# Kernel optimization log

Hardware: AMD Instinct MI355X
Metric: run time of the kernel (lower is better)

The kernel has to match this reference:

```python
import jax, jax.numpy as jnp
import numpy as np

DIM = 128
NUM_HEADS = 8
HEAD_DIM = DIM // NUM_HEADS
SCALE = HEAD_DIM ** -0.5


def _attn_branch(xs, Wq, bq, Wp, bp):
    # xs: (N, L, C) batch of sequences; Q=K=V=q (per the module)
    N, L, C = xs.shape
    q = xs @ Wq + bq                                   # (N, L, C)
    q = q.reshape(N, L, NUM_HEADS, HEAD_DIM).transpose(0, 2, 1, 3)  # (N, h, L, d)
    qs = q * SCALE
    attn = jax.nn.softmax(jnp.einsum('nhld,nhmd->nhlm', qs, qs), axis=-1)
    out = jnp.einsum('nhlm,nhmd->nhld', attn, q)       # (N, h, L, d)
    out = out.transpose(0, 2, 1, 3).reshape(N, L, C)
    return out @ Wp + bp


def setup_inputs() -> dict:
    key = jax.random.key(0)
    ks = jax.random.split(key, 12)
    B, C, D, H, W = 1, DIM, 31, 32, 32
    s = 0.02
    return {
        'x': jax.random.normal(ks[0], (B, C, D, H, W), jnp.float32),
        'Wq_spec': jax.random.normal(ks[1], (C, C), jnp.float32) * s,
        'bq_spec': jnp.zeros((C,), jnp.float32),
        'Wp_spec': jax.random.normal(ks[2], (C, C), jnp.float32) * s,
        'bp_spec': jnp.zeros((C,), jnp.float32),
        'Wq_spat': jax.random.normal(ks[3], (C, C), jnp.float32) * s,
        'bq_spat': jnp.zeros((C,), jnp.float32),
        'Wp_spat': jax.random.normal(ks[4], (C, C), jnp.float32) * s,
        'bp_spat': jnp.zeros((C,), jnp.float32),
        'Wg': jax.random.normal(ks[5], (2 * C, C), jnp.float32) * s,
        'bg': jnp.zeros((C,), jnp.float32),
    }


def reference(x, Wq_spec, bq_spec, Wp_spec, bp_spec,
              Wq_spat, bq_spat, Wp_spat, bp_spat, Wg, bg):
    B, C, D, H, W = x.shape
    # ---- spectral branch: sequences of length D per spatial position ----
    x_spec = x.transpose(0, 3, 4, 2, 1).reshape(B * H * W, D, C)
    out_spec = _attn_branch(x_spec, Wq_spec, bq_spec, Wp_spec, bp_spec)
    out_spectral = out_spec.reshape(B, H, W, D, C).transpose(0, 4, 3, 1, 2)  # (B,C,D,H,W)
    # ---- spatial branch: sequences of length H*W per band ----
    x_spat = x.transpose(0, 2, 3, 4, 1).reshape(B * D, H * W, C)
    out_spat = _attn_branch(x_spat, Wq_spat, bq_spat, Wp_spat, bp_spat)
    out_spatial = out_spat.reshape(B, D, H, W, C).transpose(0, 4, 1, 2, 3)   # (B,C,D,H,W)
    # ---- sigmoid-gated fusion (global average pooled gate) ----
    gi = jnp.concatenate([
        out_spectral.mean(axis=(2, 3, 4)),
        out_spatial.mean(axis=(2, 3, 4)),
    ], axis=-1)                                          # (B, 2C)
    gate = jax.nn.sigmoid(gi @ Wg + bg)[:, :, None, None, None]  # (B,C,1,1,1)
    return gate * out_spectral + (1.0 - gate) * out_spatial
```

## Files before the change

### kernel.cpp

```cpp
#include <hip/hip_runtime.h>
#include <cstddef>

#define CC 128
#define NH 8
#define HD 16
#define DDIM 31
#define HWW 1024
#define TOK 31744
#define SCALE2 0.0625f
#define QTOK 64

typedef __attribute__((ext_vector_type(4))) short  short4v;
typedef __attribute__((ext_vector_type(8))) short  short8v;
typedef __attribute__((ext_vector_type(4))) float  float4v;
typedef __attribute__((ext_vector_type(2))) unsigned uint2v;
typedef __attribute__((ext_vector_type(8))) __bf16 bf16x8;

__device__ inline unsigned bf16rne(float f) {
    unsigned u = __float_as_uint(f);
    return (u + 0x7fffu + ((u >> 16) & 1u)) >> 16;
}
__device__ inline float bf2f(unsigned h) { return __uint_as_float(h << 16); }

__device__ inline unsigned packsplit(float v) {
    unsigned h = bf16rne(v);
    unsigned l = bf16rne(v - bf2f(h));
    return h | (l << 16);
}
__device__ inline uint2 pack_hi4(uint4 p) {
    return make_uint2((p.x & 0xffffu) | (p.y << 16),
                      (p.z & 0xffffu) | (p.w << 16));
}
__device__ inline uint2 pack_lo4(uint4 p) {
    return make_uint2((p.x >> 16) | (p.y & 0xffff0000u),
                      (p.z >> 16) | (p.w & 0xffff0000u));
}

__device__ inline short4v pack_pf(unsigned u0, unsigned u1,
                                  unsigned u2, unsigned u3) {
    uint2v pd;
    pd[0] = __builtin_amdgcn_perm(u1, u0, 0x07060302u);
    pd[1] = __builtin_amdgcn_perm(u3, u2, 0x07060302u);
    return __builtin_bit_cast(short4v, pd);
}

__device__ inline float4v mfma32(short8v a, short8v b, float4v c) {
    return __builtin_amdgcn_mfma_f32_16x16x32_bf16(
        __builtin_bit_cast(bf16x8, a), __builtin_bit_cast(bf16x8, b), c, 0, 0, 0);
}

__device__ inline void load_wfrags32(const float* __restrict__ W, int co0, int l,
                                     int quad, short8v* ah, short8v* al)
{
#pragma unroll
    for (int k4 = 0; k4 < 4; ++k4) {
#pragma unroll
        for (int j = 0; j < 8; ++j) {
            float w = W[(size_t)(k4 * 32 + quad * 8 + j) * CC + co0 + l];
            unsigned h = bf16rne(w);
            ah[k4][j] = (short)h;
            al[k4][j] = (short)bf16rne(w - bf2f(h));
        }
    }
}

#define AST 136

__global__ __launch_bounds__(512, 4) void qproj_kernel(
    const float* __restrict__ x,
    const float* __restrict__ Wq1, const float* __restrict__ Wq2,
    const float* __restrict__ bq1, const float* __restrict__ bq2,
    unsigned* __restrict__ q1p, unsigned* __restrict__ q2p,
    float* __restrict__ sums)
{
    __shared__ ushort sbuf[2 * QTOK * AST];
    ushort* Ahi = sbuf;
    ushort* Alo = sbuf + QTOK * AST;
    unsigned* S = (unsigned*)sbuf;
    const int tid = threadIdx.x;
    const int t0  = blockIdx.x * QTOK;
    if (blockIdx.x == 0 && tid < 2 * CC) sums[tid] = 0.f;

    for (int i = tid; i < QTOK * 32; i += 512) {
        int t = i & 63, c4 = i >> 6;
        unsigned hw[2], lw[2];
#pragma unroll
        for (int p = 0; p < 2; ++p) {
            unsigned h0, l0, h1, l1;
            {
                float v = x[(size_t)(c4 * 4 + p * 2 + 0) * TOK + t0 + t];
                h0 = bf16rne(v); l0 = bf16rne(v - bf2f(h0));
            }
            {
                float v = x[(size_t)(c4 * 4 + p * 2 + 1) * TOK + t0 + t];
                h1 = bf16rne(v); l1 = bf16rne(v - bf2f(h1));
            }
            hw[p] = h0 | (h1 << 16);
            lw[p] = l0 | (l1 << 16);
        }
        *(uint2*)&Ahi[t * AST + c4 * 4] = make_uint2(hw[0], hw[1]);
        *(uint2*)&Alo[t * AST + c4 * 4] = make_uint2(lw[0], lw[1]);
    }
    __syncthreads();

    const int lane = tid & 63;
    const int l    = lane & 15;
    const int quad = lane >> 4;
    const int co0  = (tid >> 6) * 16;

    short8v ah[2][4], al[2][4];
    load_wfrags32(Wq1, co0, l, quad, ah[0], al[0]);
    load_wfrags32(Wq2, co0, l, quad, ah[1], al[1]);
    float4v acc[2][4];
#pragma unroll
    for (int br = 0; br < 2; ++br)
#pragma unroll
        for (int nt = 0; nt < 4; ++nt) acc[br][nt] = (float4v){0.f, 0.f, 0.f, 0.f};
#pragma unroll
    for (int k4 = 0; k4 < 4; ++k4) {
#pragma unroll
        for (int nt = 0; nt < 4; ++nt) {
            short8v bh = *(const short8v*)&Ahi[(nt * 16 + l) * AST + k4 * 32 + quad * 8];
            short8v bl = *(const short8v*)&Alo[(nt * 16 + l) * AST + k4 * 32 + quad * 8];
            acc[0][nt] = mfma32(ah[0][k4], bh, acc[0][nt]);
            acc[0][nt] = mfma32(ah[0][k4], bl, acc[0][nt]);
            acc[0][nt] = mfma32(al[0][k4], bh, acc[0][nt]);
            acc[1][nt] = mfma32(ah[1][k4], bh, acc[1][nt]);
            acc[1][nt] = mfma32(ah[1][k4], bl, acc[1][nt]);
            acc[1][nt] = mfma32(al[1][k4], bh, acc[1][nt]);
        }
    }

    for (int branch = 0; branch < 2; ++branch) {
        const float* bq = branch ? bq2 : bq1;
        unsigned* op    = branch ? q2p : q1p;
        float4 bv = *(const float4*)&bq[co0 + quad * 4];
        float bb[4] = {bv.x, bv.y, bv.z, bv.w};
        __syncthreads();
#pragma unroll
        for (int nt = 0; nt < 4; ++nt) {
#pragma unroll
            for (int reg = 0; reg < 4; ++reg)
                S[(nt * 16 + l) * AST + co0 + quad * 4 + reg] =
                    packsplit(acc[branch][nt][reg] + bb[reg]);
        }
        __syncthreads();
        for (int i = tid; i < QTOK * 32; i += 512) {
            int t = i >> 5, c4 = i & 31;
            uint4 pv = *(const uint4*)&S[t * AST + c4 * 4];
            *(uint4*)&op[(size_t)(t0 + t) * CC + c4 * 4] = pv;
        }
    }
}

#define QS2 132
#define QSS 20
#define QTP 1044
__global__ __launch_bounds__(1024, 4) void attn_kernel(
    unsigned* __restrict__ q1p, unsigned* __restrict__ q2p,
    float* __restrict__ sums)
{
    __shared__ __align__(16) ushort smem[HWW * QSS + HD * QTP];
    __shared__ float fsum[CC];
    const int tid  = threadIdx.x;
    const int lane = tid & 63;
    const int l    = lane & 15;
    const int quad = lane >> 4;
    const float k2 = SCALE2 * 1.44269504f;
    const short4v onesb = {(short)0x3F80, (short)0x3F80, (short)0x3F80, (short)0x3F80};
    if (tid < CC) fsum[tid] = 0.f;

    {
        const int d = blockIdx.x >> 3, h = blockIdx.x & 7;
        ushort* Qs  = smem;
        ushort* QTs = smem + HWW * QSS;
        const size_t base = (size_t)d * HWW * CC + h * HD;

        for (int i = tid; i < HWW * 4; i += 1024) {
            int row = i >> 2, q4 = i & 3;
            uint4 p = *(const uint4*)&q2p[base + (size_t)row * CC + q4 * 4];
            *(uint2*)&Qs[row * QSS + q4 * 4] = pack_hi4(p);
            QTs[(q4 * 4 + 0) * QTP + row] = (ushort)p.x;
            QTs[(q4 * 4 + 1) * QTP + row] = (ushort)p.y;
            QTs[(q4 * 4 + 2) * QTP + row] = (ushort)p.z;
            QTs[(q4 * 4 + 3) * QTP + row] = (ushort)p.w;
        }
        __syncthreads();

        const int Rw = (tid >> 6) * 64;
        short4v qf[4];
#pragma unroll
        for (int lt = 0; lt < 4; ++lt) {
            short4v raw = *(short4v*)&Qs[(Rw + lt * 16 + l) * QSS + quad * 4];
            short4v sc;
#pragma unroll
            for (int e = 0; e < 4; ++e) {
                float f = bf2f((unsigned)(ushort)raw[e]) * k2;
                sc[e] = (short)bf16rne(f);
            }
            qf[lt] = sc;
        }

        float4v acc[4], accs[4];
#pragma unroll
        for (int lt = 0; lt < 4; ++lt) {
            acc[lt]  = (float4v){0.f, 0.f, 0.f, 0.f};
            accs[lt] = (float4v){0.f, 0.f, 0.f, 0.f};
        }

#pragma unroll 2
        for (int mt = 0; mt < 64; ++mt) {
            const int m0 = mt * 16;
            short4v ka = *(short4v*)&Qs[(m0 + l) * QSS + quad * 4];
            short4v vb = *(short4v*)&QTs[l * QTP + m0 + quad * 4];
#pragma unroll
            for (int lt = 0; lt < 4; ++lt) {
                float4v s = __builtin_amdgcn_mfma_f32_16x16x16bf16_1k(
                    ka, qf[lt], (float4v){0.f, 0.f, 0.f, 0.f}, 0, 0, 0);
                unsigned u0 = __float_as_uint(__builtin_amdgcn_exp2f(s[0]));
                unsigned u1 = __float_as_uint(__builtin_amdgcn_exp2f(s[1]));
                unsigned u2 = __float_as_uint(__builtin_amdgcn_exp2f(s[2]));
                unsigned u3 = __float_as_uint(__builtin_amdgcn_exp2f(s[3]));
                short4v pf = pack_pf(u0, u1, u2, u3);
                acc[lt]  = __builtin_amdgcn_mfma_f32_16x16x16bf16_1k(vb, pf, acc[lt], 0, 0, 0);
                accs[lt] = __builtin_amdgcn_mfma_f32_16x16x16bf16_1k(onesb, pf, accs[lt], 0, 0, 0);
            }
        }

        float vsum[4] = {0.f, 0.f, 0.f, 0.f};
#pragma unroll
        for (int lt = 0; lt < 4; ++lt) {
            float inv = 1.f / accs[lt][0];
            int token = Rw + lt * 16 + l;
            float v0 = acc[lt][0] * inv, v1 = acc[lt][1] * inv;
            float v2 = acc[lt][2] * inv, v3 = acc[lt][3] * inv;
            uint4 pv;
            pv.x = packsplit(v0); pv.y = packsplit(v1);
            pv.z = packsplit(v2); pv.w = packsplit(v3);
            *(uint4*)&q2p[base + (size_t)token * CC + quad * 4] = pv;
            vsum[0] += v0; vsum[1] += v1; vsum[2] += v2; vsum[3] += v3;
        }
#pragma unroll
        for (int reg = 0; reg < 4; ++reg) {
            float v = vsum[reg];
            v += __shfl_xor(v, 1); v += __shfl_xor(v, 2);
            v += __shfl_xor(v, 4); v += __shfl_xor(v, 8);
            if (l == 0) atomicAdd(&fsum[quad * 4 + reg], v);
        }
        __syncthreads();
        if (tid < HD) atomicAdd(&sums[CC + h * HD + tid], fsum[tid]);
    }

    const int half_id = blockIdx.x >> 1;
    const bool has_job = (blockIdx.x & 1) ? (half_id < 4) : (half_id < 124);
    if (!has_job) return;
    const int job = (blockIdx.x & 1) ? (124 + half_id) : half_id;
    const int hw0 = job * 8;

    __syncthreads();
    if (tid < CC) fsum[tid] = 0.f;

    const int wave = tid >> 6;
    const int hwl  = wave >> 1;
    const int half = wave & 1;
    const int hw   = hw0 + hwl;
    ushort* Q = smem + hwl * (32 * QS2);
    for (int it = 0; it < 8; ++it) {
        int idx = it * 64 + lane;
        int dd = half * 16 + (idx >> 5), c4 = idx & 31;
        if (dd < 31) {
            uint4 p = *(const uint4*)&q1p[((size_t)dd * HWW + hw) * CC + c4 * 4];
            *(uint2*)&Q[dd * QS2 + c4 * 4] = pack_hi4(p);
        }
    }
    if (half) for (int i = lane; i < 128; i += 64) Q[31 * QS2 + i] = 0;
    __syncthreads();

    const int hh = half * 4;
#pragma unroll
    for (int hl = 0; hl < 4; ++hl) {
        const int hc = (hh + hl) * HD;
        short4v qf[2];
        qf[0] = *(const short4v*)&Q[l * QS2 + hc + quad * 4];
        qf[1] = *(const short4v*)&Q[(16 + l) * QS2 + hc + quad * 4];
        short4v va[2];
#pragma unroll
        for (int j = 0; j < 2; ++j)
#pragma unroll
            for (int jj = 0; jj < 4; ++jj)
                va[j][jj] = (short)Q[(j * 16 + quad * 4 + jj) * QS2 + hc + l];

        float4v o[2]   = {(float4v){0.f,0.f,0.f,0.f}, (float4v){0.f,0.f,0.f,0.f}};
        float4v osr[2] = {(float4v){0.f,0.f,0.f,0.f}, (float4v){0.f,0.f,0.f,0.f}};
#pragma unroll
        for (int j = 0; j < 2; ++j) {
#pragma unroll
            for (int i2 = 0; i2 < 2; ++i2) {
                float4v s = __builtin_amdgcn_mfma_f32_16x16x16bf16_1k(
                    qf[j], qf[i2], (float4v){0.f,0.f,0.f,0.f}, 0, 0, 0);
                unsigned u0 = __float_as_uint(__builtin_amdgcn_exp2f(s[0] * k2));
                unsigned u1 = __float_as_uint(__builtin_amdgcn_exp2f(s[1] * k2));
                unsigned u2 = __float_as_uint(__builtin_amdgcn_exp2f(s[2] * k2));
                unsigned u3 = __float_as_uint(__builtin_amdgcn_exp2f(s[3] * k2));
                if (j == 1 && quad == 3) u3 = 0;
                short4v pf = pack_pf(u0, u1, u2, u3);
                o[i2]   = __builtin_amdgcn_mfma_f32_16x16x16bf16_1k(va[j], pf, o[i2], 0, 0, 0);
                osr[i2] = __builtin_amdgcn_mfma_f32_16x16x16bf16_1k(onesb, pf, osr[i2], 0, 0, 0);
            }
        }
        float vsum[4] = {0.f, 0.f, 0.f, 0.f};
#pragma unroll
        for (int i2 = 0; i2 < 2; ++i2) {
            float inv = 1.f / osr[i2][0];
            int dq = i2 * 16 + l;
            if (dq < 31) {
                uint4 pv;
                float v0 = o[i2][0] * inv, v1 = o[i2][1] * inv;
                float v2 = o[i2][2] * inv, v3 = o[i2][3] * inv;
                pv.x = packsplit(v0); pv.y = packsplit(v1);
                pv.z = packsplit(v2); pv.w = packsplit(v3);
                *(uint4*)&q1p[((size_t)dq * HWW + hw) * CC + hc + quad * 4] = pv;
                vsum[0] += v0; vsum[1] += v1; vsum[2] += v2; vsum[3] += v3;
            }
        }
#pragma unroll
        for (int r = 0; r < 4; ++r) {
            float v = vsum[r];
            v += __shfl_xor(v, 1); v += __shfl_xor(v, 2);
            v += __shfl_xor(v, 4); v += __shfl_xor(v, 8);
            if (l == 0) atomicAdd(&fsum[hc + quad * 4 + r], v);
        }
    }
    __syncthreads();
    if (tid < CC) atomicAdd(&sums[tid], fsum[tid]);
}

__global__ __launch_bounds__(512, 4) void oproj_kernel(
    const unsigned* __restrict__ q1p, const unsigned* __restrict__ q2p,
    const float* __restrict__ Wp1, const float* __restrict__ Wp2,
    const float* __restrict__ bp1, const float* __restrict__ bp2,
    const float* __restrict__ Wg,  const float* __restrict__ bg,
    const float* __restrict__ sums, float* __restrict__ out)
{
    __shared__ ushort sbuf[2 * 64 * AST];
    ushort* Ahi = sbuf;
    ushort* Alo = sbuf + 64 * AST;
    unsigned* S = (unsigned*)sbuf;
    __shared__ float pa[4][CC];
    __shared__ float giv[2 * CC];
    __shared__ float gf[CC];
    const int tid = threadIdx.x;
    const int t0  = blockIdx.x * 64;
    const int lane = tid & 63;
    const int l    = lane & 15;
    const int quad = lane >> 4;
    const int co0  = (tid >> 6) * 16;

    {
        const int part = tid >> 7, c = tid & 127;
        const float* Wp = (part < 2) ? Wp1 : Wp2;
        const float* sp = (part < 2) ? sums : sums + CC;
        const int k0 = (part & 1) * 64;
        float a = 0.f;
        for (int kk = 0; kk < 64; ++kk) {
            int k = k0 + kk;
            a += sp[k] * Wp[(size_t)k * CC + c];
        }
        pa[part][c] = a;
        __syncthreads();
        if (tid < 2 * CC) {
            float m = (tid < CC) ? (pa[0][tid] + pa[1][tid])
                                 : (pa[2][tid - CC] + pa[3][tid - CC]);
            float bb = (tid < CC) ? bp1[tid] : bp2[tid - CC];
            giv[tid] = m * (1.f / (float)TOK) + bb;
        }
        __syncthreads();
        float b = 0.f;
        for (int kk = 0; kk < 64; ++kk) {
            int j = part * 64 + kk;
            b += giv[j] * Wg[(size_t)j * CC + c];
        }
        pa[part][c] = b;
        __syncthreads();
        if (tid < CC)
            gf[tid] = 1.f / (1.f + __expf(-(bg[tid] + pa[0][tid] + pa[1][tid] +
                                           pa[2][tid] + pa[3][tid])));
    }

    float4v acc[2][4];
#pragma unroll
    for (int br = 0; br < 2; ++br)
#pragma unroll
        for (int nt = 0; nt < 4; ++nt) acc[br][nt] = (float4v){0.f, 0.f, 0.f, 0.f};

    for (int br = 0; br < 2; ++br) {
        const unsigned* Ap = br ? q2p : q1p;
        const float*    W  = br ? Wp2 : Wp1;
        short8v ah[4], al[4];
        load_wfrags32(W, co0, l, quad, ah, al);
        __syncthreads();
        for (int i = tid; i < 64 * 32; i += 512) {
            int t = i >> 5, c4 = i & 31;
            uint4 p = *(const uint4*)&Ap[(size_t)(t0 + t) * CC + c4 * 4];
            *(uint2*)&Ahi[t * AST + c4 * 4] = pack_hi4(p);
            *(uint2*)&Alo[t * AST + c4 * 4] = pack_lo4(p);
        }
        __syncthreads();
#pragma unroll
        for (int k4 = 0; k4 < 4; ++k4) {
#pragma unroll
            for (int nt = 0; nt < 4; ++nt) {
                short8v bh = *(const short8v*)&Ahi[(nt * 16 + l) * AST + k4 * 32 + quad * 8];
                short8v bl = *(const short8v*)&Alo[(nt * 16 + l) * AST + k4 * 32 + quad * 8];
                acc[br][nt] = mfma32(ah[k4], bh, acc[br][nt]);
                acc[br][nt] = mfma32(ah[k4], bl, acc[br][nt]);
                acc[br][nt] = mfma32(al[k4], bh, acc[br][nt]);
            }
        }
    }

    float4 b1 = *(const float4*)&bp1[co0 + quad * 4];
    float4 b2 = *(const float4*)&bp2[co0 + quad * 4];
    float bb1[4] = {b1.x, b1.y, b1.z, b1.w};
    float bb2[4] = {b2.x, b2.y, b2.z, b2.w};
    float gg[4];
#pragma unroll
    for (int e = 0; e < 4; ++e) gg[e] = gf[co0 + quad * 4 + e];

    __syncthreads();
#pragma unroll
    for (int nt = 0; nt < 4; ++nt) {
        int tl = nt * 16 + l;
#pragma unroll
        for (int reg = 0; reg < 4; ++reg) {
            float v = gg[reg] * (acc[0][nt][reg] + bb1[reg]) +
                      (1.f - gg[reg]) * (acc[1][nt][reg] + bb2[reg]);
            S[(co0 + quad * 4 + reg) * 66 + tl] = __float_as_uint(v);
        }
    }
    __syncthreads();
    for (int i = tid; i < 128 * 32; i += 512) {
        int co = i >> 5, t2 = i & 31;
        uint2 v = *(const uint2*)&S[co * 66 + t2 * 2];
        *(uint2*)&out[(size_t)co * TOK + t0 + t2 * 2] = v;
    }
}

extern "C" void kernel_launch(void* const* d_in, const int* in_sizes, int n_in,
                              void* d_out, int out_size, void* d_ws, size_t ws_size,
                              hipStream_t stream)
{
    const float* x   = (const float*)d_in[0];
    const float* Wq1 = (const float*)d_in[1];
    const float* bq1 = (const float*)d_in[2];
    const float* Wp1 = (const float*)d_in[3];
    const float* bp1 = (const float*)d_in[4];
    const float* Wq2 = (const float*)d_in[5];
    const float* bq2 = (const float*)d_in[6];
    const float* Wp2 = (const float*)d_in[7];
    const float* bp2 = (const float*)d_in[8];
    const float* Wg  = (const float*)d_in[9];
    const float* bg  = (const float*)d_in[10];
    float* out = (float*)d_out;

    const size_t plane = (size_t)TOK * CC;
    unsigned* q1p = (unsigned*)d_ws;
    unsigned* q2p = q1p + plane;
    float*   sums = (float*)(q2p + plane);

    const size_t need = 2 * plane * sizeof(unsigned) + 2 * CC * sizeof(float);
    if (ws_size < need) return;

    qproj_kernel<<<dim3(TOK / QTOK), 512, 0, stream>>>(x, Wq1, Wq2, bq1, bq2,
                                                       q1p, q2p, sums);
    attn_kernel<<<dim3(248), 1024, 0, stream>>>(q1p, q2p, sums);
    oproj_kernel<<<dim3(496), 512, 0, stream>>>(q1p, q2p,
                                                Wp1, Wp2, bp1, bp2, Wg, bg,
                                                sums, out);
}
```

Before: 172.0 us.

## Store Q projections as bf16-only buffers and split attention blocks by branch

The Q projection now writes only the high bf16 half into separate 16-bit workspace buffers, where it used to write packed hi/lo pairs. This halves the bytes qproj stores and attn reads, since attention only ever used the high part. The attention kernel no longer runs both branches in every block. It launches 376 blocks: the first 128 handle spectral sequences and the rest handle spatial ones, which removes the uneven tail job assignment. The cost is extra workspace for the two new buffers, and each block now does a single, shorter task.

New measurement: 159.9 us. 7.1% less time.

```diff
diff --git a/kernel.cpp b/kernel.cpp
--- a/kernel.cpp
+++ b/kernel.cpp
@@ -70,13 +70,12 @@
     const float* __restrict__ x,
     const float* __restrict__ Wq1, const float* __restrict__ Wq2,
     const float* __restrict__ bq1, const float* __restrict__ bq2,
-    unsigned* __restrict__ q1p, unsigned* __restrict__ q2p,
+    ushort* __restrict__ qh1, ushort* __restrict__ qh2,
     float* __restrict__ sums)
 {
     __shared__ ushort sbuf[2 * QTOK * AST];
     ushort* Ahi = sbuf;
     ushort* Alo = sbuf + QTOK * AST;
-    unsigned* S = (unsigned*)sbuf;
     const int tid = threadIdx.x;
     const int t0  = blockIdx.x * QTOK;
     if (blockIdx.x == 0 && tid < 2 * CC) sums[tid] = 0.f;
@@ -131,25 +130,26 @@
         }
     }
 
-    for (int branch = 0; branch < 2; ++branch) {
-        const float* bq = branch ? bq2 : bq1;
-        unsigned* op    = branch ? q2p : q1p;
-        float4 bv = *(const float4*)&bq[co0 + quad * 4];
-        float bb[4] = {bv.x, bv.y, bv.z, bv.w};
-        __syncthreads();
-#pragma unroll
-        for (int nt = 0; nt < 4; ++nt) {
+    float4 bv1 = *(const float4*)&bq1[co0 + quad * 4];
+    float4 bv2 = *(const float4*)&bq2[co0 + quad * 4];
+    float bb[2][4] = {{bv1.x, bv1.y, bv1.z, bv1.w},
+                      {bv2.x, bv2.y, bv2.z, bv2.w}};
+    __syncthreads();
+#pragma unroll
+    for (int br = 0; br < 2; ++br)
+#pragma unroll
+        for (int nt = 0; nt < 4; ++nt)
 #pragma unroll
             for (int reg = 0; reg < 4; ++reg)
-                S[(nt * 16 + l) * AST + co0 + quad * 4 + reg] =
-                    packsplit(acc[branch][nt][reg] + bb[reg]);
-        }
-        __syncthreads();
-        for (int i = tid; i < QTOK * 32; i += 512) {
-            int t = i >> 5, c4 = i & 31;
-            uint4 pv = *(const uint4*)&S[t * AST + c4 * 4];
-            *(uint4*)&op[(size_t)(t0 + t) * CC + c4 * 4] = pv;
-        }
+                sbuf[br * (QTOK * AST) + (nt * 16 + l) * AST + co0 + quad * 4 + reg] =
+                    (ushort)bf16rne(acc[br][nt][reg] + bb[br][reg]);
+    __syncthreads();
+    for (int i = tid; i < 2 * QTOK * 16; i += 512) {
+        int br = i >> 10, j = i & 1023;
+        int t = j >> 4, c8 = j & 15;
+        ushort* op = br ? qh2 : qh1;
+        uint4 pv = *(const uint4*)&sbuf[br * (QTOK * AST) + t * AST + c8 * 8];
+        *(uint4*)&op[(size_t)(t0 + t) * CC + c8 * 8] = pv;
     }
 }
 
@@ -157,6 +157,7 @@
 #define QSS 20
 #define QTP 1044
 __global__ __launch_bounds__(1024, 4) void attn_kernel(
+    const ushort* __restrict__ qh1, const ushort* __restrict__ qh2,
     unsigned* __restrict__ q1p, unsigned* __restrict__ q2p,
     float* __restrict__ sums)
 {
@@ -170,20 +171,23 @@
     const short4v onesb = {(short)0x3F80, (short)0x3F80, (short)0x3F80, (short)0x3F80};
     if (tid < CC) fsum[tid] = 0.f;
 
-    {
-        const int d = blockIdx.x >> 3, h = blockIdx.x & 7;
+    if (blockIdx.x >= 128) {
+        const int sp = blockIdx.x - 128;
+        const int d = sp >> 3, h = sp & 7;
         ushort* Qs  = smem;
         ushort* QTs = smem + HWW * QSS;
-        const size_t base = (size_t)d * HWW * CC + h * HD;
+        const size_t baseh = (size_t)d * HWW * CC + h * HD;
+        const size_t base  = baseh;
 
         for (int i = tid; i < HWW * 4; i += 1024) {
             int row = i >> 2, q4 = i & 3;
-            uint4 p = *(const uint4*)&q2p[base + (size_t)row * CC + q4 * 4];
-            *(uint2*)&Qs[row * QSS + q4 * 4] = pack_hi4(p);
-            QTs[(q4 * 4 + 0) * QTP + row] = (ushort)p.x;
-            QTs[(q4 * 4 + 1) * QTP + row] = (ushort)p.y;
-            QTs[(q4 * 4 + 2) * QTP + row] = (ushort)p.z;
-            QTs[(q4 * 4 + 3) * QTP + row] = (ushort)p.w;
+            uint2 p = *(const uint2*)&qh2[baseh + (size_t)row * CC + q4 * 4];
+            *(uint2*)&Qs[row * QSS + q4 * 4] = p;
+            const ushort* ps = (const ushort*)&p;
+            QTs[(q4 * 4 + 0) * QTP + row] = ps[0];
+            QTs[(q4 * 4 + 1) * QTP + row] = ps[1];
+            QTs[(q4 * 4 + 2) * QTP + row] = ps[2];
+            QTs[(q4 * 4 + 3) * QTP + row] = ps[3];
         }
         __syncthreads();
 
@@ -249,90 +253,82 @@
         }
         __syncthreads();
         if (tid < HD) atomicAdd(&sums[CC + h * HD + tid], fsum[tid]);
-    }
-
-    const int half_id = blockIdx.x >> 1;
-    const bool has_job = (blockIdx.x & 1) ? (half_id < 4) : (half_id < 124);
-    if (!has_job) return;
-    const int job = (blockIdx.x & 1) ? (124 + half_id) : half_id;
-    const int hw0 = job * 8;
-
-    __syncthreads();
-    if (tid < CC) fsum[tid] = 0.f;
-
-    const int wave = tid >> 6;
-    const int hwl  = wave >> 1;
-    const int half = wave & 1;
-    const int hw   = hw0 + hwl;
-    ushort* Q = smem + hwl * (32 * QS2);
-    for (int it = 0; it < 8; ++it) {
-        int idx = it * 64 + lane;
-        int dd = half * 16 + (idx >> 5), c4 = idx & 31;
-        if (dd < 31) {
-            uint4 p = *(const uint4*)&q1p[((size_t)dd * HWW + hw) * CC + c4 * 4];
-            *(uint2*)&Q[dd * QS2 + c4 * 4] = pack_hi4(p);
-        }
-    }
-    if (half) for (int i = lane; i < 128; i += 64) Q[31 * QS2 + i] = 0;
-    __syncthreads();
-
-    const int hh = half * 4;
-#pragma unroll
-    for (int hl = 0; hl < 4; ++hl) {
-        const int hc = (hh + hl) * HD;
-        short4v qf[2];
-        qf[0] = *(const short4v*)&Q[l * QS2 + hc + quad * 4];
-        qf[1] = *(const short4v*)&Q[(16 + l) * QS2 + hc + quad * 4];
-        short4v va[2];
-#pragma unroll
-        for (int j = 0; j < 2; ++j)
-#pragma unroll
-            for (int jj = 0; jj < 4; ++jj)
-                va[j][jj] = (short)Q[(j * 16 + quad * 4 + jj) * QS2 + hc + l];
-
-        float4v o[2]   = {(float4v){0.f,0.f,0.f,0.f}, (float4v){0.f,0.f,0.f,0.f}};
-        float4v osr[2] = {(float4v){0.f,0.f,0.f,0.f}, (float4v){0.f,0.f,0.f,0.f}};
-#pragma unroll
-        for (int j = 0; j < 2; ++j) {
+    } else {
+        const int hw0 = blockIdx.x * 8;
+        const int wave = tid >> 6;
+        const int hwl  = wave >> 1;
+        const int half = wave & 1;
+        const int hw   = hw0 + hwl;
+        ushort* Q = smem + hwl * (32 * QS2);
+        for (int it = 0; it < 8; ++it) {
+            int idx = it * 64 + lane;
+            int dd = half * 16 + (idx >> 5), c4 = idx & 31;
+            if (dd < 31) {
+                uint2 p = *(const uint2*)&qh1[((size_t)dd * HWW + hw) * CC + c4 * 4];
+                *(uint2*)&Q[dd * QS2 + c4 * 4] = p;
+            }
+        }
+        if (half) for (int i = lane; i < 128; i += 64) Q[31 * QS2 + i] = 0;
+        __syncthreads();
+
+        const int hh = half * 4;
+#pragma unroll
+        for (int hl = 0; hl < 4; ++hl) {
+            const int hc = (hh + hl) * HD;
+            short4v qf[2];
+            qf[0] = *(const short4v*)&Q[l * QS2 + hc + quad * 4];
+            qf[1] = *(const short4v*)&Q[(16 + l) * QS2 + hc + quad * 4];
+            short4v va[2];
+#pragma unroll
+            for (int j = 0; j < 2; ++j)
+#pragma unroll
+                for (int jj = 0; jj < 4; ++jj)
+                    va[j][jj] = (short)Q[(j * 16 + quad * 4 + jj) * QS2 + hc + l];
+
+            float4v o[2]   = {(float4v){0.f,0.f,0.f,0.f}, (float4v){0.f,0.f,0.f,0.f}};
+            float4v osr[2] = {(float4v){0.f,0.f,0.f,0.f}, (float4v){0.f,0.f,0.f,0.f}};
+#pragma unroll
+            for (int j = 0; j < 2; ++j) {
+#pragma unroll
+                for (int i2 = 0; i2 < 2; ++i2) {
+                    float4v s = __builtin_amdgcn_mfma_f32_16x16x16bf16_1k(
+                        qf[j], qf[i2], (float4v){0.f,0.f,0.f,0.f}, 0, 0, 0);
+                    unsigned u0 = __float_as_uint(__builtin_amdgcn_exp2f(s[0] * k2));
+                    unsigned u1 = __float_as_uint(__builtin_amdgcn_exp2f(s[1] * k2));
+                    unsigned u2 = __float_as_uint(__builtin_amdgcn_exp2f(s[2] * k2));
+                    unsigned u3 = __float_as_uint(__builtin_amdgcn_exp2f(s[3] * k2));
+                    if (j == 1 && quad == 3) u3 = 0;
+                    short4v pf = pack_pf(u0, u1, u2, u3);
+                    o[i2]   = __builtin_amdgcn_mfma_f32_16x16x16bf16_1k(va[j], pf, o[i2], 0, 0, 0);
+                    osr[i2] = __builtin_amdgcn_mfma_f32_16x16x16bf16_1k(onesb, pf, osr[i2], 0, 0, 0);
+                }
+            }
+            float vsum[4] = {0.f, 0.f, 0.f, 0.f};
 #pragma unroll
             for (int i2 = 0; i2 < 2; ++i2) {
-                float4v s = __builtin_amdgcn_mfma_f32_16x16x16bf16_1k(
-                    qf[j], qf[i2], (float4v){0.f,0.f,0.f,0.f}, 0, 0, 0);
-                unsigned u0 = __float_as_uint(__builtin_amdgcn_exp2f(s[0] * k2));
-                unsigned u1 = __float_as_uint(__builtin_amdgcn_exp2f(s[1] * k2));
-                unsigned u2 = __float_as_uint(__builtin_amdgcn_exp2f(s[2] * k2));
-                unsigned u3 = __float_as_uint(__builtin_amdgcn_exp2f(s[3] * k2));
-                if (j == 1 && quad == 3) u3 = 0;
-                short4v pf = pack_pf(u0, u1, u2, u3);
-                o[i2]   = __builtin_amdgcn_mfma_f32_16x16x16bf16_1k(va[j], pf, o[i2], 0, 0, 0);
-                osr[i2] = __builtin_amdgcn_mfma_f32_16x16x16bf16_1k(onesb, pf, osr[i2], 0, 0, 0);
-            }
-        }
-        float vsum[4] = {0.f, 0.f, 0.f, 0.f};
-#pragma unroll
-        for (int i2 = 0; i2 < 2; ++i2) {
-            float inv = 1.f / osr[i2][0];
-            int dq = i2 * 16 + l;
-            if (dq < 31) {
-                uint4 pv;
-                float v0 = o[i2][0] * inv, v1 = o[i2][1] * inv;
-                float v2 = o[i2][2] * inv, v3 = o[i2][3] * inv;
-                pv.x = packsplit(v0); pv.y = packsplit(v1);
-                pv.z = packsplit(v2); pv.w = packsplit(v3);
-                *(uint4*)&q1p[((size_t)dq * HWW + hw) * CC + hc + quad * 4] = pv;
-                vsum[0] += v0; vsum[1] += v1; vsum[2] += v2; vsum[3] += v3;
-            }
-        }
-#pragma unroll
-        for (int r = 0; r < 4; ++r) {
-            float v = vsum[r];
-            v += __shfl_xor(v, 1); v += __shfl_xor(v, 2);
-            v += __shfl_xor(v, 4); v += __shfl_xor(v, 8);
-            if (l == 0) atomicAdd(&fsum[hc + quad * 4 + r], v);
-        }
-    }
-    __syncthreads();
-    if (tid < CC) atomicAdd(&sums[tid], fsum[tid]);
+                float inv = 1.f / osr[i2][0];
+                int dq = i2 * 16 + l;
+                if (dq < 31) {
+                    uint4 pv;
+                    float v0 = o[i2][0] * inv, v1 = o[i2][1] * inv;
+                    float v2 = o[i2][2] * inv, v3 = o[i2][3] * inv;
+                    pv.x = packsplit(v0); pv.y = packsplit(v1);
+                    pv.z = packsplit(v2); pv.w = packsplit(v3);
+                    *(uint4*)&q1p[((size_t)dq * HWW + hw) * CC + hc + quad * 4] = pv;
+                    vsum[0] += v0; vsum[1] += v1; vsum[2] += v2; vsum[3] += v3;
+                }
+            }
+#pragma unroll
+            for (int r = 0; r < 4; ++r) {
+                float v = vsum[r];
+                v += __shfl_xor(v, 1); v += __shfl_xor(v, 2);
+                v += __shfl_xor(v, 4); v += __shfl_xor(v, 8);
+                if (l == 0) atomicAdd(&fsum[hc + quad * 4 + r], v);
+            }
+        }
+        __syncthreads();
+        if (tid < CC) atomicAdd(&sums[tid], fsum[tid]);
+    }
 }
 
 __global__ __launch_bounds__(512, 4) void oproj_kernel(
@@ -466,14 +462,17 @@
     const size_t plane = (size_t)TOK * CC;
     unsigned* q1p = (unsigned*)d_ws;
     unsigned* q2p = q1p + plane;
-    float*   sums = (float*)(q2p + plane);
-
-    const size_t need = 2 * plane * sizeof(unsigned) + 2 * CC * sizeof(float);
+    ushort*  qh1  = (ushort*)(q2p + plane);
+    ushort*  qh2  = qh1 + plane;
+    float*   sums = (float*)(qh2 + plane);
+
+    const size_t need = 2 * plane * sizeof(unsigned) + 2 * plane * sizeof(ushort) +
+                        2 * CC * sizeof(float);
     if (ws_size < need) return;
 
     qproj_kernel<<<dim3(TOK / QTOK), 512, 0, stream>>>(x, Wq1, Wq2, bq1, bq2,
-                                                       q1p, q2p, sums);
-    attn_kernel<<<dim3(248), 1024, 0, stream>>>(q1p, q2p, sums);
+                                                       qh1, qh2, sums);
+    attn_kernel<<<dim3(376), 1024, 0, stream>>>(qh1, qh2, q1p, q2p, sums);
     oproj_kernel<<<dim3(496), 512, 0, stream>>>(q1p, q2p,
                                                 Wp1, Wp2, bp1, bp2, Wg, bg,
                                                 sums, out);
```
